# Kernel optimization log

Hardware: AMD Instinct MI355X
Metric: run time of the kernel (lower is better)

## Reference

```python
import jax, jax.numpy as jnp
import numpy as np

C_IN = 256
RED = 8
C_QK = C_IN // RED  # 32


def setup_inputs() -> dict:
    key = jax.random.key(0)
    ks = jax.random.split(key, 7)
    B, C, H, W = 4, C_IN, 64, 64
    s = 1.0 / np.sqrt(C)
    return {
        "x": jax.random.normal(ks[0], (B, C, H, W), dtype=jnp.float32),
        "wq": jax.random.uniform(ks[1], (C_QK, C), jnp.float32, -s, s),
        "bq": jax.random.uniform(ks[2], (C_QK,), jnp.float32, -s, s),
        "wk": jax.random.uniform(ks[3], (C_QK, C), jnp.float32, -s, s),
        "bk": jax.random.uniform(ks[4], (C_QK,), jnp.float32, -s, s),
        "wv": jax.random.uniform(ks[5], (C, C), jnp.float32, -s, s),
        "bv": jax.random.uniform(ks[6], (C,), jnp.float32, -s, s),
        "gamma": jnp.zeros((1,), dtype=jnp.float32),
    }


def reference(x, wq, bq, wk, bk, wv, bv, gamma):
    B, C, H, W = x.shape
    N = H * W
    xf = x.reshape(B, C, N)  # flatten spatial tokens
    # 1x1 convs == per-pixel linear projections over channels
    q = jnp.einsum("oc,bcn->bno", wq, xf) + bq            # (B, N, C_qk)
    k = jnp.einsum("oc,bcn->bon", wk, xf) + bk[:, None]   # (B, C_qk, N)
    v = jnp.einsum("oc,bcn->bon", wv, xf) + bv[:, None]   # (B, C, N)
    # unscaled attention: softmax over keys (last dim)
    attn = jax.nn.softmax(jnp.einsum("bio,boj->bij", q, k), axis=-1)  # (B, N, N)
    # attended[b,c,i] = sum_j v[b,c,j] * attn[b,i,j]  (bmm with attn^T)
    attended = jnp.einsum("bcj,bij->bci", v, attn).reshape(B, C, H, W)
    output = gamma[0] * attended + x
    attention_map = attn.mean(axis=1).reshape(B, H, W)
    return output, attention_map
```

## Files before the change

### kernel.cpp

```cpp
#include <hip/hip_runtime.h>


#define B_   4
#define C_   256
#define N_   4096
#define CQK_ 32
#define BCN_ (B_*C_*N_)
#define BN_  (B_*N_)
#define TP_  260
#define LOG2E 1.4426950408889634f

typedef __attribute__((ext_vector_type(8))) short short8v;
typedef __attribute__((ext_vector_type(4))) short short4v;
typedef __attribute__((ext_vector_type(4))) float f32x4;
typedef unsigned short ushort_t;

__device__ __forceinline__ ushort_t f2bf(float f) {
  unsigned u = __builtin_bit_cast(unsigned, f);
  u += 0x7FFFu + ((u >> 16) & 1u);
  return (ushort_t)(u >> 16);
}
__device__ __forceinline__ float bf2f(ushort_t h) {
  unsigned u = ((unsigned)h) << 16;
  return __builtin_bit_cast(float, u);
}
__device__ __forceinline__ short8v ld8f(const float* p) {
  float4 a = *(const float4*)p, b = *(const float4*)(p + 4);
  short8v r;
  r[0]=f2bf(a.x); r[1]=f2bf(a.y); r[2]=f2bf(a.z); r[3]=f2bf(a.w);
  r[4]=f2bf(b.x); r[5]=f2bf(b.y); r[6]=f2bf(b.z); r[7]=f2bf(b.w);
  return r;
}
__device__ __forceinline__ short8v ld8lds(const ushort_t* p) {
  short4v lo = *(const short4v*)p, hi = *(const short4v*)(p + 4);
  return __builtin_shufflevector(lo, hi, 0, 1, 2, 3, 4, 5, 6, 7);
}

__global__ __launch_bounds__(256) void
k_prep(const float* __restrict__ x,
       const float* __restrict__ wq, const float* __restrict__ bq,
       const float* __restrict__ wk, const float* __restrict__ bk,
       const float* __restrict__ wv, const float* __restrict__ bv,
       const float* __restrict__ gamma,
       float* __restrict__ out, float* __restrict__ l,
       ushort_t* __restrict__ qb, ushort_t* __restrict__ kb,
       float* __restrict__ v_t) {
  __shared__ ushort_t xs[32 * TP_];
  int blk = blockIdx.x, tid = threadIdx.x;
  int b = blk >> 7, n0 = (blk & 127) << 5;
#pragma unroll
  for (int it = 0; it < 8; ++it) {
    int flat = it * 256 + tid;
    int c = flat >> 3, t4 = flat & 7;
    size_t off = ((size_t)(b * C_) + c) * N_ + n0 + t4 * 4;
    float4 v = *(const float4*)(x + off);
    *(float4*)(out + off) = v;
    ushort_t* dst = &xs[(t4 * 4) * TP_ + c];
    dst[0]        = f2bf(v.x);
    dst[TP_]      = f2bf(v.y);
    dst[2 * TP_]  = f2bf(v.z);
    dst[3 * TP_]  = f2bf(v.w);
  }
  if (blk < 64) {
    int idx = blk * 256 + tid;
    l[idx] = 0.0f;
    out[BCN_ + idx] = 0.0f;
  }
  __syncthreads();

  int wave = tid >> 6, lane = tid & 63;
  int col16 = lane & 15, quad = lane >> 4;
  int g = wave & 1;
  bool isq = wave < 2;
  int tok_l = g * 16 + col16;
  int n = n0 + tok_l;
  short8v bfr[8];
#pragma unroll
  for (int ks = 0; ks < 8; ++ks)
    bfr[ks] = ld8lds(&xs[tok_l * TP_ + ks * 32 + quad * 8]);

  const float* wrow = isq ? wq : wk;
  const float* bias = isq ? bq : bk;
  ushort_t* dst = isq ? qb : kb;
#pragma unroll
  for (int mt = 0; mt < 2; ++mt) {
    f32x4 c = {0.f, 0.f, 0.f, 0.f};
#pragma unroll
    for (int ks = 0; ks < 8; ++ks) {
      short8v afr = ld8f(wrow + (mt * 16 + col16) * C_ + ks * 32 + quad * 8);
      c = __builtin_amdgcn_mfma_f32_16x16x32_bf16(afr, bfr[ks], c, 0, 0, 0);
    }
    int co = mt * 16 + quad * 4;
    ushort4 pk;
    if (isq) {
      pk.x = f2bf((c[0] + bias[co + 0]) * LOG2E);
      pk.y = f2bf((c[1] + bias[co + 1]) * LOG2E);
      pk.z = f2bf((c[2] + bias[co + 2]) * LOG2E);
      pk.w = f2bf((c[3] + bias[co + 3]) * LOG2E);
    } else {
      pk.x = f2bf(c[0] + bias[co + 0]); pk.y = f2bf(c[1] + bias[co + 1]);
      pk.z = f2bf(c[2] + bias[co + 2]); pk.w = f2bf(c[3] + bias[co + 3]);
    }
    *(ushort4*)(dst + ((size_t)(b * N_) + n) * CQK_ + co) = pk;
  }

  if (gamma[0] != 0.0f) {
    int half = wave >> 1;
    for (int vt = 0; vt < 8; ++vt) {
      int tile = half * 8 + vt;
      f32x4 c = {0.f, 0.f, 0.f, 0.f};
#pragma unroll
      for (int ks = 0; ks < 8; ++ks) {
        short8v afr = ld8f(wv + (tile * 16 + col16) * C_ + ks * 32 + quad * 8);
        c = __builtin_amdgcn_mfma_f32_16x16x32_bf16(afr, bfr[ks], c, 0, 0, 0);
      }
      int co = tile * 16 + quad * 4;
      float4 o;
      o.x = c[0] + bv[co];     o.y = c[1] + bv[co + 1];
      o.z = c[2] + bv[co + 2]; o.w = c[3] + bv[co + 3];
      *(float4*)(v_t + ((size_t)(b * N_) + n) * C_ + co) = o;
    }
  }
}

__global__ __launch_bounds__(256) void
k_rowsA(const ushort_t* __restrict__ qb, const ushort_t* __restrict__ kb,
        float* __restrict__ l) {
  int blk = blockIdx.x;
  int b = blk >> 8, rg = (blk >> 2) & 63, js = blk & 3;
  int wave = threadIdx.x >> 6, lane = threadIdx.x & 63;
  int col16 = lane & 15, quad = lane >> 4;
  const ushort_t* qbb = qb + (size_t)b * N_ * CQK_;
  const ushort_t* kbb = kb + (size_t)b * N_ * CQK_;
  int i_base = rg * 64;
  short8v a[4];
#pragma unroll
  for (int t = 0; t < 4; ++t)
    a[t] = *(const short8v*)(qbb + (i_base + t * 16 + col16) * CQK_ + quad * 8);
  float racc[16];
#pragma unroll
  for (int r = 0; r < 16; ++r) racc[r] = 0.0f;
  int j_base = js * 1024 + wave * 256;
#pragma unroll 4
  for (int t = 0; t < 16; ++t) {
    short8v bfr = *(const short8v*)(kbb + (j_base + t * 16 + col16) * CQK_ + quad * 8);
#pragma unroll
    for (int m = 0; m < 4; ++m) {
      f32x4 c = {0.f, 0.f, 0.f, 0.f};
      c = __builtin_amdgcn_mfma_f32_16x16x32_bf16(a[m], bfr, c, 0, 0, 0);
      racc[m * 4 + 0] += __builtin_amdgcn_exp2f(c[0]);
      racc[m * 4 + 1] += __builtin_amdgcn_exp2f(c[1]);
      racc[m * 4 + 2] += __builtin_amdgcn_exp2f(c[2]);
      racc[m * 4 + 3] += __builtin_amdgcn_exp2f(c[3]);
    }
  }
#pragma unroll
  for (int r = 0; r < 16; ++r) {
    float v = racc[r];
    v += __shfl_xor(v, 1); v += __shfl_xor(v, 2);
    v += __shfl_xor(v, 4); v += __shfl_xor(v, 8);
    racc[r] = v;
  }
  if (col16 == 0) {
    float* lb = l + b * N_ + i_base;
#pragma unroll
    for (int m = 0; m < 4; ++m)
#pragma unroll
      for (int rr = 0; rr < 4; ++rr)
        atomicAdd(&lb[m * 16 + quad * 4 + rr], racc[m * 4 + rr]);
  }
}

__global__ __launch_bounds__(256) void
k_mapB(const ushort_t* __restrict__ qb, const ushort_t* __restrict__ kb,
       const float* __restrict__ l, float* __restrict__ map) {
  int blk = blockIdx.x;
  int b = blk >> 8, jg = (blk >> 4) & 15, isp = blk & 15;
  int wave = threadIdx.x >> 6, lane = threadIdx.x & 63;
  int col16 = lane & 15, quad = lane >> 4;
  const ushort_t* qbb = qb + (size_t)b * N_ * CQK_;
  const ushort_t* kbb = kb + (size_t)b * N_ * CQK_;
  int j_base = jg * 256 + wave * 64;
  short8v a[4];
#pragma unroll
  for (int t = 0; t < 4; ++t)
    a[t] = *(const short8v*)(kbb + (j_base + t * 16 + col16) * CQK_ + quad * 8);
  float csum[16];
#pragma unroll
  for (int r = 0; r < 16; ++r) csum[r] = 0.0f;
  int i_base = isp * 256;
#pragma unroll 4
  for (int t = 0; t < 16; ++t) {
    int i0 = i_base + t * 16;
    short8v bfr = *(const short8v*)(qbb + (i0 + col16) * CQK_ + quad * 8);
    float llog = -__builtin_amdgcn_logf(l[b * N_ + i0 + col16]);
    f32x4 cinit = {llog, llog, llog, llog};
#pragma unroll
    for (int m = 0; m < 4; ++m) {
      f32x4 c = __builtin_amdgcn_mfma_f32_16x16x32_bf16(a[m], bfr, cinit, 0, 0, 0);
      csum[m * 4 + 0] += __builtin_amdgcn_exp2f(c[0]);
      csum[m * 4 + 1] += __builtin_amdgcn_exp2f(c[1]);
      csum[m * 4 + 2] += __builtin_amdgcn_exp2f(c[2]);
      csum[m * 4 + 3] += __builtin_amdgcn_exp2f(c[3]);
    }
  }
#pragma unroll
  for (int r = 0; r < 16; ++r) {
    float v = csum[r];
    v += __shfl_xor(v, 1); v += __shfl_xor(v, 2);
    v += __shfl_xor(v, 4); v += __shfl_xor(v, 8);
    csum[r] = v;
  }
  if (col16 == 0) {
    float* mp = map + b * N_ + j_base;
#pragma unroll
    for (int m = 0; m < 4; ++m)
#pragma unroll
      for (int rr = 0; rr < 4; ++rr)
        atomicAdd(&mp[m * 16 + quad * 4 + rr], csum[m * 4 + rr] * (1.0f / (float)N_));
  }
}

__global__ __launch_bounds__(256) void
k_pv(const ushort_t* __restrict__ qb, const ushort_t* __restrict__ kb,
     const float* __restrict__ v_t, const float* __restrict__ l,
     const float* __restrict__ gamma, float* __restrict__ out) {
  if (gamma[0] == 0.0f) return;
  __shared__ float qs[32 * CQK_];
  __shared__ float invl[32];
  __shared__ float ps[32 * 256];
  int blk = blockIdx.x;
  int b = blk >> 9, i0 = ((blk >> 2) & 127) << 5, jsp = blk & 3;
  int tid = threadIdx.x;
  for (int r = tid; r < 32 * CQK_; r += 256)
    qs[r] = bf2f(qb[((size_t)(b * N_) + i0) * CQK_ + r]);
  if (tid < 32) invl[tid] = 1.0f / l[b * N_ + i0 + tid];
  __syncthreads();
  float g = gamma[0];
  float acc[32];
#pragma unroll
  for (int i = 0; i < 32; ++i) acc[i] = 0.0f;
  for (int jt = jsp * 4; jt < jsp * 4 + 4; ++jt) {
    int j = jt * 256 + tid;
    const ushort_t* krow = kb + ((size_t)(b * N_) + j) * CQK_;
    float kcol[CQK_];
#pragma unroll
    for (int o = 0; o < CQK_; ++o) kcol[o] = bf2f(krow[o]);
#pragma unroll
    for (int i = 0; i < 32; ++i) {
      float s = 0.0f;
#pragma unroll
      for (int o = 0; o < CQK_; ++o) s += qs[i * CQK_ + o] * kcol[o];
      ps[i * 256 + tid] = __builtin_amdgcn_exp2f(s) * invl[i];
    }
    __syncthreads();
    const float* vtb = v_t + ((size_t)(b * N_) + jt * 256) * C_;
    for (int jj = 0; jj < 256; ++jj) {
      float vv = vtb[(size_t)jj * C_ + tid];
#pragma unroll
      for (int i = 0; i < 32; ++i) acc[i] += ps[i * 256 + jj] * vv;
    }
    __syncthreads();
  }
  float* ob = out + ((size_t)(b * C_) + tid) * N_ + i0;
#pragma unroll
  for (int i = 0; i < 32; ++i) atomicAdd(&ob[i], g * acc[i]);
}

extern "C" void kernel_launch(void* const* d_in, const int* in_sizes, int n_in,
                              void* d_out, int out_size, void* d_ws, size_t ws_size,
                              hipStream_t stream) {
  const float* x     = (const float*)d_in[0];
  const float* wq    = (const float*)d_in[1];
  const float* bq    = (const float*)d_in[2];
  const float* wk    = (const float*)d_in[3];
  const float* bk    = (const float*)d_in[4];
  const float* wv    = (const float*)d_in[5];
  const float* bv    = (const float*)d_in[6];
  const float* gamma = (const float*)d_in[7];
  float* out = (float*)d_out;
  float* wsf = (float*)d_ws;
  float*    l   = wsf;
  ushort_t* qb  = (ushort_t*)(wsf + 16384);
  ushort_t* kb  = (ushort_t*)(wsf + 16384 + 262144);
  float*    v_t = wsf + 16384 + 2 * 262144;

  k_prep <<< 512, 256, 0, stream>>>(x, wq, bq, wk, bk, wv, bv, gamma,
                                    out, l, qb, kb, v_t);
  k_rowsA<<<1024, 256, 0, stream>>>(qb, kb, l);
  k_mapB <<<1024, 256, 0, stream>>>(qb, kb, l, out + BCN_);
  k_pv   <<<2048, 256, 0, stream>>>(qb, kb, v_t, l, gamma, out);
}
```

Baseline: 122.5 us.

## Fuse four attention kernels into one cooperative kernel with grid syncs

Merges the prep, row-sum, attention-map and PV kernels into a single cooperative launch of 512 blocks that separates phases with grid.sync(), falling back to the split kernels if the cooperative launch fails. The goal is to remove per-launch overhead and the gaps between kernels. Each block now does twice the work in the A and B phases, and fewer blocks run than before, which may lower latency hiding. The PV phase is split into 16-row halves.

```diff
diff --git a/kernel.cpp b/kernel.cpp
--- a/kernel.cpp
+++ b/kernel.cpp
@@ -1,4 +1,7 @@
 #include <hip/hip_runtime.h>
+#include <hip/hip_cooperative_groups.h>
+
+namespace cg = cooperative_groups;
 
 
 #define B_   4
@@ -9,6 +12,7 @@
 #define BN_  (B_*N_)
 #define TP_  260
 #define LOG2E 1.4426950408889634f
+#define SMEM_BYTES 18560
 
 typedef __attribute__((ext_vector_type(8))) short short8v;
 typedef __attribute__((ext_vector_type(4))) short short4v;
@@ -36,17 +40,14 @@
   return __builtin_shufflevector(lo, hi, 0, 1, 2, 3, 4, 5, 6, 7);
 }
 
-__global__ __launch_bounds__(256) void
-k_prep(const float* __restrict__ x,
-       const float* __restrict__ wq, const float* __restrict__ bq,
-       const float* __restrict__ wk, const float* __restrict__ bk,
-       const float* __restrict__ wv, const float* __restrict__ bv,
-       const float* __restrict__ gamma,
+__device__ __forceinline__ void
+phaseP(const float* __restrict__ x, const float* __restrict__ wq,
+       const float* __restrict__ bq, const float* __restrict__ wk,
+       const float* __restrict__ bk, const float* __restrict__ wv,
+       const float* __restrict__ bv, float g0,
        float* __restrict__ out, float* __restrict__ l,
        ushort_t* __restrict__ qb, ushort_t* __restrict__ kb,
-       float* __restrict__ v_t) {
-  __shared__ ushort_t xs[32 * TP_];
-  int blk = blockIdx.x, tid = threadIdx.x;
+       float* __restrict__ v_t, ushort_t* xs, int blk, int tid) {
   int b = blk >> 7, n0 = (blk & 127) << 5;
 #pragma unroll
   for (int it = 0; it < 8; ++it) {
@@ -56,10 +57,10 @@
     float4 v = *(const float4*)(x + off);
     *(float4*)(out + off) = v;
     ushort_t* dst = &xs[(t4 * 4) * TP_ + c];
-    dst[0]        = f2bf(v.x);
-    dst[TP_]      = f2bf(v.y);
-    dst[2 * TP_]  = f2bf(v.z);
-    dst[3 * TP_]  = f2bf(v.w);
+    dst[0]       = f2bf(v.x);
+    dst[TP_]     = f2bf(v.y);
+    dst[2 * TP_] = f2bf(v.z);
+    dst[3 * TP_] = f2bf(v.w);
   }
   if (blk < 64) {
     int idx = blk * 256 + tid;
@@ -104,7 +105,7 @@
     *(ushort4*)(dst + ((size_t)(b * N_) + n) * CQK_ + co) = pk;
   }
 
-  if (gamma[0] != 0.0f) {
+  if (g0 != 0.0f) {
     int half = wave >> 1;
     for (int vt = 0; vt < 8; ++vt) {
       int tile = half * 8 + vt;
@@ -123,16 +124,13 @@
   }
 }
 
-__global__ __launch_bounds__(256) void
-k_rowsA(const ushort_t* __restrict__ qb, const ushort_t* __restrict__ kb,
-        float* __restrict__ l) {
-  int blk = blockIdx.x;
-  int b = blk >> 8, rg = (blk >> 2) & 63, js = blk & 3;
-  int wave = threadIdx.x >> 6, lane = threadIdx.x & 63;
+__device__ __forceinline__ void
+phaseA(const ushort_t* __restrict__ qb, const ushort_t* __restrict__ kb,
+       float* __restrict__ l, int b, int i_base, int j0, int tcnt, int tid) {
+  int wave = tid >> 6, lane = tid & 63;
   int col16 = lane & 15, quad = lane >> 4;
   const ushort_t* qbb = qb + (size_t)b * N_ * CQK_;
   const ushort_t* kbb = kb + (size_t)b * N_ * CQK_;
-  int i_base = rg * 64;
   short8v a[4];
 #pragma unroll
   for (int t = 0; t < 4; ++t)
@@ -140,9 +138,9 @@
   float racc[16];
 #pragma unroll
   for (int r = 0; r < 16; ++r) racc[r] = 0.0f;
-  int j_base = js * 1024 + wave * 256;
+  int j_base = j0 + wave * (tcnt * 16);
 #pragma unroll 4
-  for (int t = 0; t < 16; ++t) {
+  for (int t = 0; t < tcnt; ++t) {
     short8v bfr = *(const short8v*)(kbb + (j_base + t * 16 + col16) * CQK_ + quad * 8);
 #pragma unroll
     for (int m = 0; m < 4; ++m) {
@@ -171,12 +169,11 @@
   }
 }
 
-__global__ __launch_bounds__(256) void
-k_mapB(const ushort_t* __restrict__ qb, const ushort_t* __restrict__ kb,
-       const float* __restrict__ l, float* __restrict__ map) {
-  int blk = blockIdx.x;
-  int b = blk >> 8, jg = (blk >> 4) & 15, isp = blk & 15;
-  int wave = threadIdx.x >> 6, lane = threadIdx.x & 63;
+__device__ __forceinline__ void
+phaseB(const ushort_t* __restrict__ qb, const ushort_t* __restrict__ kb,
+       const float* __restrict__ l, float* __restrict__ map,
+       int b, int jg, int i_base, int tcnt, int tid) {
+  int wave = tid >> 6, lane = tid & 63;
   int col16 = lane & 15, quad = lane >> 4;
   const ushort_t* qbb = qb + (size_t)b * N_ * CQK_;
   const ushort_t* kbb = kb + (size_t)b * N_ * CQK_;
@@ -188,9 +185,8 @@
   float csum[16];
 #pragma unroll
   for (int r = 0; r < 16; ++r) csum[r] = 0.0f;
-  int i_base = isp * 256;
 #pragma unroll 4
-  for (int t = 0; t < 16; ++t) {
+  for (int t = 0; t < tcnt; ++t) {
     int i0 = i_base + t * 16;
     short8v bfr = *(const short8v*)(qbb + (i0 + col16) * CQK_ + quad * 8);
     float llog = -__builtin_amdgcn_logf(l[b * N_ + i0 + col16]);
@@ -221,33 +217,30 @@
   }
 }
 
-__global__ __launch_bounds__(256) void
-k_pv(const ushort_t* __restrict__ qb, const ushort_t* __restrict__ kb,
-     const float* __restrict__ v_t, const float* __restrict__ l,
-     const float* __restrict__ gamma, float* __restrict__ out) {
-  if (gamma[0] == 0.0f) return;
-  __shared__ float qs[32 * CQK_];
-  __shared__ float invl[32];
-  __shared__ float ps[32 * 256];
-  int blk = blockIdx.x;
-  int b = blk >> 9, i0 = ((blk >> 2) & 127) << 5, jsp = blk & 3;
-  int tid = threadIdx.x;
-  for (int r = tid; r < 32 * CQK_; r += 256)
+__device__ __forceinline__ void
+phasePV(const ushort_t* __restrict__ qb, const ushort_t* __restrict__ kb,
+        const float* __restrict__ v_t, const float* __restrict__ l, float g,
+        float* __restrict__ out, int b, int i0, int jt_lo, int jt_hi,
+        char* smem, int tid) {
+  float* qs   = (float*)smem;
+  float* invl = (float*)(smem + 2048);
+  float* ps   = (float*)(smem + 2176);
+  __syncthreads();
+  for (int r = tid; r < 16 * CQK_; r += 256)
     qs[r] = bf2f(qb[((size_t)(b * N_) + i0) * CQK_ + r]);
-  if (tid < 32) invl[tid] = 1.0f / l[b * N_ + i0 + tid];
+  if (tid < 16) invl[tid] = 1.0f / l[b * N_ + i0 + tid];
   __syncthreads();
-  float g = gamma[0];
-  float acc[32];
-#pragma unroll
-  for (int i = 0; i < 32; ++i) acc[i] = 0.0f;
-  for (int jt = jsp * 4; jt < jsp * 4 + 4; ++jt) {
+  float acc[16];
+#pragma unroll
+  for (int i = 0; i < 16; ++i) acc[i] = 0.0f;
+  for (int jt = jt_lo; jt < jt_hi; ++jt) {
     int j = jt * 256 + tid;
     const ushort_t* krow = kb + ((size_t)(b * N_) + j) * CQK_;
     float kcol[CQK_];
 #pragma unroll
     for (int o = 0; o < CQK_; ++o) kcol[o] = bf2f(krow[o]);
 #pragma unroll
-    for (int i = 0; i < 32; ++i) {
+    for (int i = 0; i < 16; ++i) {
       float s = 0.0f;
 #pragma unroll
       for (int o = 0; o < CQK_; ++o) s += qs[i * CQK_ + o] * kcol[o];
@@ -258,13 +251,89 @@
     for (int jj = 0; jj < 256; ++jj) {
       float vv = vtb[(size_t)jj * C_ + tid];
 #pragma unroll
-      for (int i = 0; i < 32; ++i) acc[i] += ps[i * 256 + jj] * vv;
+      for (int i = 0; i < 16; ++i) acc[i] += ps[i * 256 + jj] * vv;
     }
     __syncthreads();
   }
   float* ob = out + ((size_t)(b * C_) + tid) * N_ + i0;
 #pragma unroll
-  for (int i = 0; i < 32; ++i) atomicAdd(&ob[i], g * acc[i]);
+  for (int i = 0; i < 16; ++i) atomicAdd(&ob[i], g * acc[i]);
+}
+
+__global__ __launch_bounds__(256, 4) void
+k_fused(const float* __restrict__ x,
+        const float* __restrict__ wq, const float* __restrict__ bq,
+        const float* __restrict__ wk, const float* __restrict__ bk,
+        const float* __restrict__ wv, const float* __restrict__ bv,
+        const float* __restrict__ gamma,
+        float* __restrict__ out, float* __restrict__ l,
+        ushort_t* __restrict__ qb, ushort_t* __restrict__ kb,
+        float* __restrict__ v_t) {
+  __shared__ __align__(16) char smem[SMEM_BYTES];
+  cg::grid_group grid = cg::this_grid();
+  int blk = blockIdx.x, tid = threadIdx.x;
+  float g0 = gamma[0];
+
+  phaseP(x, wq, bq, wk, bk, wv, bv, g0, out, l, qb, kb, v_t,
+         (ushort_t*)smem, blk, tid);
+  grid.sync();
+  {
+    int b = blk >> 7, rem = blk & 127;
+    phaseA(qb, kb, l, b, (rem >> 1) * 64, (rem & 1) * 2048, 32, tid);
+  }
+  grid.sync();
+  {
+    int b = blk >> 7, rem = blk & 127;
+    phaseB(qb, kb, l, out + BCN_, b, rem >> 3, (rem & 7) * 512, 32, tid);
+  }
+  if (g0 != 0.0f) {
+    int b = blk >> 7, rem = blk & 127;
+    for (int it2 = 0; it2 < 2; ++it2)
+      phasePV(qb, kb, v_t, l, g0, out, b, rem * 32 + it2 * 16, 0, 16, smem, tid);
+  }
+}
+
+__global__ __launch_bounds__(256) void
+k_prepS(const float* __restrict__ x, const float* __restrict__ wq,
+        const float* __restrict__ bq, const float* __restrict__ wk,
+        const float* __restrict__ bk, const float* __restrict__ wv,
+        const float* __restrict__ bv, const float* __restrict__ gamma,
+        float* __restrict__ out, float* __restrict__ l,
+        ushort_t* __restrict__ qb, ushort_t* __restrict__ kb,
+        float* __restrict__ v_t) {
+  __shared__ __align__(16) char smem[32 * TP_ * 2];
+  phaseP(x, wq, bq, wk, bk, wv, bv, gamma[0], out, l, qb, kb, v_t,
+         (ushort_t*)smem, blockIdx.x, threadIdx.x);
+}
+
+__global__ __launch_bounds__(256) void
+k_rowsS(const ushort_t* __restrict__ qb, const ushort_t* __restrict__ kb,
+        float* __restrict__ l) {
+  int blk = blockIdx.x;
+  phaseA(qb, kb, l, blk >> 8, ((blk >> 2) & 63) * 64, (blk & 3) * 1024, 16,
+         threadIdx.x);
+}
+
+__global__ __launch_bounds__(256) void
+k_mapS(const ushort_t* __restrict__ qb, const ushort_t* __restrict__ kb,
+       const float* __restrict__ l, float* __restrict__ map) {
+  int blk = blockIdx.x;
+  phaseB(qb, kb, l, map, blk >> 8, (blk >> 4) & 15, (blk & 15) * 256, 16,
+         threadIdx.x);
+}
+
+__global__ __launch_bounds__(256) void
+k_pvS(const ushort_t* __restrict__ qb, const ushort_t* __restrict__ kb,
+      const float* __restrict__ v_t, const float* __restrict__ l,
+      const float* __restrict__ gamma, float* __restrict__ out) {
+  float g = gamma[0];
+  if (g == 0.0f) return;
+  __shared__ __align__(16) char smem[SMEM_BYTES];
+  int blk = blockIdx.x;
+  int b = blk >> 9, rem = (blk >> 2) & 127, jsp = blk & 3;
+  for (int it2 = 0; it2 < 2; ++it2)
+    phasePV(qb, kb, v_t, l, g, out, b, rem * 32 + it2 * 16,
+            jsp * 4, jsp * 4 + 4, smem, threadIdx.x);
 }
 
 extern "C" void kernel_launch(void* const* d_in, const int* in_sizes, int n_in,
@@ -285,9 +354,16 @@
   ushort_t* kb  = (ushort_t*)(wsf + 16384 + 262144);
   float*    v_t = wsf + 16384 + 2 * 262144;
 
-  k_prep <<< 512, 256, 0, stream>>>(x, wq, bq, wk, bk, wv, bv, gamma,
-                                    out, l, qb, kb, v_t);
-  k_rowsA<<<1024, 256, 0, stream>>>(qb, kb, l);
-  k_mapB <<<1024, 256, 0, stream>>>(qb, kb, l, out + BCN_);
-  k_pv   <<<2048, 256, 0, stream>>>(qb, kb, v_t, l, gamma, out);
-}
+  void* args[] = {(void*)&x, (void*)&wq, (void*)&bq, (void*)&wk, (void*)&bk,
+                  (void*)&wv, (void*)&bv, (void*)&gamma, (void*)&out,
+                  (void*)&l, (void*)&qb, (void*)&kb, (void*)&v_t};
+  hipError_t err = hipLaunchCooperativeKernel((const void*)k_fused, dim3(512),
+                                              dim3(256), args, 0, stream);
+  if (err != hipSuccess) {
+    k_prepS<<< 512, 256, 0, stream>>>(x, wq, bq, wk, bk, wv, bv, gamma,
+                                      out, l, qb, kb, v_t);
+    k_rowsS<<<1024, 256, 0, stream>>>(qb, kb, l);
+    k_mapS <<<1024, 256, 0, stream>>>(qb, kb, l, out + BCN_);
+    k_pvS  <<<2048, 256, 0, stream>>>(qb, kb, v_t, l, gamma, out);
+  }
+}
```

New measurement: 236.8 us. 1.93x slower.
